# Performance work log

Measured on AMD Instinct MI355X. Metric: run time of the kernel, lower is better.

The kernel has to match this reference:

```python
import jax, jax.numpy as jnp
import numpy as np

DIM = 768
HEADS = 12
HEAD_DIM = DIM // HEADS
MLP_DIM = 4 * DIM
EPS = 1e-5


def setup_inputs() -> dict:
    key = jax.random.key(0)
    ks = jax.random.split(key, 8)
    s = lambda fan_in: 1.0 / np.sqrt(fan_in)
    return {
        "x": jax.random.normal(ks[0], (2, 2048, DIM), dtype=jnp.float32),
        "ln1_w": jnp.ones((DIM,), jnp.float32),
        "ln1_b": jnp.zeros((DIM,), jnp.float32),
        # weights stored [in, out]
        "qkv_w": jax.random.normal(ks[1], (DIM, 3 * DIM), jnp.float32) * s(DIM),
        "qkv_b": jnp.zeros((3 * DIM,), jnp.float32),
        "proj_w": jax.random.normal(ks[2], (DIM, DIM), jnp.float32) * s(DIM),
        "proj_b": jnp.zeros((DIM,), jnp.float32),
        "ln2_w": jnp.ones((DIM,), jnp.float32),
        "ln2_b": jnp.zeros((DIM,), jnp.float32),
        "lin1_w": jax.random.normal(ks[3], (DIM, MLP_DIM), jnp.float32) * s(DIM),
        "lin1_b": jnp.zeros((MLP_DIM,), jnp.float32),
        "lin2_w": jax.random.normal(ks[4], (MLP_DIM, DIM), jnp.float32) * s(MLP_DIM),
        "lin2_b": jnp.zeros((DIM,), jnp.float32),
    }


def _layernorm(x, w, b):
    mu = jnp.mean(x, axis=-1, keepdims=True)
    var = jnp.mean(jnp.square(x - mu), axis=-1, keepdims=True)
    return (x - mu) * jax.lax.rsqrt(var + EPS) * w + b


def _attention(x, qkv_w, qkv_b, proj_w, proj_b):
    B, N, C = x.shape
    qkv = (x @ qkv_w + qkv_b).reshape(B, N, 3, HEADS, HEAD_DIM)
    q, k, v = qkv[:, :, 0], qkv[:, :, 1], qkv[:, :, 2]  # [B, N, H, Dh]
    scale = HEAD_DIM ** -0.5
    attn = jnp.einsum("bqhd,bkhd->bhqk", q, k) * scale  # full NxN scores
    attn = jax.nn.softmax(attn, axis=-1)
    out = jnp.einsum("bhqk,bkhd->bqhd", attn, v).reshape(B, N, C)
    return out @ proj_w + proj_b


def reference(x, ln1_w, ln1_b, qkv_w, qkv_b, proj_w, proj_b,
              ln2_w, ln2_b, lin1_w, lin1_b, lin2_w, lin2_b):
    x = x + _attention(_layernorm(x, ln1_w, ln1_b), qkv_w, qkv_b, proj_w, proj_b)
    h = _layernorm(x, ln2_w, ln2_b)
    h = jax.nn.gelu(h @ lin1_w + lin1_b, approximate=False) @ lin2_w + lin2_b
    return x + h
```

## Files before the change

kernel.cpp:

```cpp
#include <hip/hip_runtime.h>
#include <hip/hip_bf16.h>
#include <math.h>

#define DIM 768
#define NTOK 4096
#define SEQ 2048
#define HEADS 12
#define HD 64

using bf16x8 = __attribute__((ext_vector_type(8))) __bf16;
using bf16x4 = __attribute__((ext_vector_type(4))) __bf16;
using short4v = __attribute__((ext_vector_type(4))) short;
using f32x4  = __attribute__((ext_vector_type(4))) float;
typedef unsigned short u16;

#define KEXPF 0.18033688011112042f

__device__ inline u16 f2bf(float f) {
  union { float f; unsigned u; } v; v.f = f;
  unsigned r = v.u + 0x7fffu + ((v.u >> 16) & 1u);
  return (u16)(r >> 16);
}

__device__ inline void pk2bf(float a, float b, u16* o0, u16* o1) {
  union { __hip_bfloat162 h; u16 u[2]; } cv;
  cv.h = __float22bfloat162_rn(make_float2(a, b));
  *o0 = cv.u[0];
  *o1 = cv.u[1];
}

__device__ inline unsigned pku32(float a, float b) {
  union { __hip_bfloat162 h; unsigned u; } cv;
  cv.h = __float22bfloat162_rn(make_float2(a, b));
  return cv.u;
}

__device__ inline float gelu_t(float x) {
  float z = x * (1.5957691216f + 0.0713548162f * x * x);
  return x / (1.0f + __expf(-z));
}

__device__ inline void gl_lds16(const u16* g, u16* l) {
  __builtin_amdgcn_global_load_lds(
      (const __attribute__((address_space(1))) unsigned int*)g,
      (__attribute__((address_space(3))) unsigned int*)l, 16, 0, 0);
}

__global__ __launch_bounds__(256) void ln_kernel(const float* __restrict__ x,
                                                 const float* __restrict__ w,
                                                 const float* __restrict__ b,
                                                 u16* __restrict__ y) {
  int row = blockIdx.x;
  int t = threadIdx.x;
  const float* xr = x + (size_t)row * DIM;
  float v0 = xr[t], v1 = xr[t + 256], v2 = xr[t + 512];
  float s = v0 + v1 + v2;
  float q = v0 * v0 + v1 * v1 + v2 * v2;
  for (int o = 32; o > 0; o >>= 1) {
    s += __shfl_down(s, o, 64);
    q += __shfl_down(q, o, 64);
  }
  __shared__ float ws_[4], wq_[4], mb[2];
  int wid = t >> 6;
  if ((t & 63) == 0) { ws_[wid] = s; wq_[wid] = q; }
  __syncthreads();
  if (t == 0) {
    float S = ws_[0] + ws_[1] + ws_[2] + ws_[3];
    float Q = wq_[0] + wq_[1] + wq_[2] + wq_[3];
    float mean = S * (1.0f / DIM);
    float var = Q * (1.0f / DIM) - mean * mean;
    mb[0] = mean;
    mb[1] = rsqrtf(var + 1e-5f);
  }
  __syncthreads();
  float mean = mb[0], rstd = mb[1];
  u16* yr = y + (size_t)row * DIM;
  yr[t]       = f2bf((v0 - mean) * rstd * w[t]       + b[t]);
  yr[t + 256] = f2bf((v1 - mean) * rstd * w[t + 256] + b[t + 256]);
  yr[t + 512] = f2bf((v2 - mean) * rstd * w[t + 512] + b[t + 512]);
}

__global__ __launch_bounds__(256) void redln_kernel(
    const float* __restrict__ P0, const float* __restrict__ P1,
    const float* __restrict__ bias, const float* __restrict__ res,
    float* __restrict__ x2, const float* __restrict__ lnw,
    const float* __restrict__ lnb, u16* __restrict__ y) {
  int row = blockIdx.x;
  int t = threadIdx.x;
  size_t off = (size_t)row * DIM;
  float v[3];
#pragma unroll
  for (int k = 0; k < 3; ++k) {
    int c = t + k * 256;
    v[k] = P0[off + c] + P1[off + c] + bias[c] + res[off + c];
    x2[off + c] = v[k];
  }
  float s = v[0] + v[1] + v[2];
  float q = v[0] * v[0] + v[1] * v[1] + v[2] * v[2];
  for (int o = 32; o > 0; o >>= 1) {
    s += __shfl_down(s, o, 64);
    q += __shfl_down(q, o, 64);
  }
  __shared__ float ws_[4], wq_[4], mb[2];
  int wid = t >> 6;
  if ((t & 63) == 0) { ws_[wid] = s; wq_[wid] = q; }
  __syncthreads();
  if (t == 0) {
    float S = ws_[0] + ws_[1] + ws_[2] + ws_[3];
    float Q = wq_[0] + wq_[1] + wq_[2] + wq_[3];
    float mean = S * (1.0f / DIM);
    float var = Q * (1.0f / DIM) - mean * mean;
    mb[0] = mean;
    mb[1] = rsqrtf(var + 1e-5f);
  }
  __syncthreads();
  float mean = mb[0], rstd = mb[1];
#pragma unroll
  for (int k = 0; k < 3; ++k) {
    int c = t + k * 256;
    y[off + c] = f2bf((v[k] - mean) * rstd * lnw[c] + lnb[c]);
  }
}

__global__ __launch_bounds__(256) void wcvt_all(
    const float* __restrict__ W0, const float* __restrict__ W1,
    const float* __restrict__ W2, const float* __restrict__ W3,
    u16* __restrict__ T0, u16* __restrict__ T1,
    u16* __restrict__ T2, u16* __restrict__ T3) {
  int id = blockIdx.x;
  const float* W; u16* Wt; int K, N, local;
  if (id < 1728)      { W = W0; Wt = T0; K = 768;  N = 2304; local = id; }
  else if (id < 2304) { W = W1; Wt = T1; K = 768;  N = 768;  local = id - 1728; }
  else if (id < 4608) { W = W2; Wt = T2; K = 768;  N = 3072; local = id - 2304; }
  else                { W = W3; Wt = T3; K = 3072; N = 768;  local = id - 4608; }
  int ntiles = N / 32;
  int n0 = (local % ntiles) * 32, k0 = (local / ntiles) * 32;
  __shared__ float tile[32][33];
  int tid = threadIdx.x;
  int c = tid & 31, r8 = tid >> 5;
#pragma unroll
  for (int p = 0; p < 4; ++p) {
    int k = r8 + p * 8;
    tile[k][c] = W[(size_t)(k0 + k) * N + n0 + c];
  }
  __syncthreads();
#pragma unroll
  for (int p = 0; p < 4; ++p) {
    int n = r8 + p * 8;
    Wt[(size_t)(n0 + n) * K + k0 + c] = f2bf(tile[c][n]);
  }
}

__global__ __launch_bounds__(256) void vtr_kernel(const u16* __restrict__ qkvB,
                                                  u16* __restrict__ vT) {
  __shared__ u16 tile[32][33];
  int v0 = blockIdx.x * 32, j0 = blockIdx.y * 32, b = blockIdx.z;
  int tid = threadIdx.x;
  int c = tid & 31, r8 = tid >> 5;
#pragma unroll
  for (int p = 0; p < 4; ++p) {
    int r = r8 + p * 8;
    tile[r][c] = qkvB[((size_t)(b * SEQ + j0 + r)) * 2304 + 1536 + v0 + c];
  }
  __syncthreads();
#pragma unroll
  for (int p = 0; p < 4; ++p) {
    int r = r8 + p * 8;
    vT[((size_t)(b * 768 + v0 + r)) * SEQ + j0 + c] = tile[c][r];
  }
}

__global__ __launch_bounds__(256) void bgemm_kernel(
    const u16* __restrict__ A, const u16* __restrict__ Bt,
    const float* __restrict__ bias, u16* __restrict__ Cb,
    int M, int N, int K, int act, int scaleq) {
  __shared__ __align__(16) u16 Asl[3][128 * 32];
  __shared__ __align__(16) u16 Bsl[3][128 * 32];
  int nwg = gridDim.x * gridDim.y;
  int bid = blockIdx.y * gridDim.x + blockIdx.x;
  int swz = (bid & 7) * (nwg >> 3) + (bid >> 3);
  int bx = swz % gridDim.x, by = swz / gridDim.x;
  int tid = threadIdx.x;
  int lane = tid & 63, wave = tid >> 6;
  int wm = wave >> 1, wn = wave & 1;
  int bm = by * 128, bn = bx * 128;
  int l15 = lane & 15, quad = lane >> 4;
  int srow4 = lane >> 2;
  int gux = (lane & 3) ^ ((srow4 + (srow4 >> 2)) & 3);

  f32x4 acc[4][4] = {};
  const u16* Ap = A + (size_t)(bm + wave * 16 + srow4) * K + gux * 8;
  const u16* Bp = Bt + (size_t)(bn + wave * 16 + srow4) * K + gux * 8;
  int fx = (l15 + (l15 >> 2)) & 3;
  int nk = K >> 5;

  auto STAGE = [&](int k0, int sel) {
#pragma unroll
    for (int p = 0; p < 2; ++p)
      gl_lds16(Ap + (size_t)(p * 64) * K + k0, &Asl[sel][(wave * 16 + p * 64) * 32]);
#pragma unroll
    for (int p = 0; p < 2; ++p)
      gl_lds16(Bp + (size_t)(p * 64) * K + k0, &Bsl[sel][(wave * 16 + p * 64) * 32]);
  };

  STAGE(0, 0);
  STAGE(32, 1);
  STAGE(64, 2);
  asm volatile("s_waitcnt vmcnt(8)" ::: "memory");
  __builtin_amdgcn_s_barrier();

  int sel = 0;
  for (int t = 0; t < nk; ++t) {
    bf16x8 af[4], bfr[4];
#pragma unroll
    for (int i = 0; i < 4; ++i) {
      af[i]  = *(const bf16x8*)&Asl[sel][(wm * 64 + i * 16 + l15) * 32 + (quad ^ fx) * 8];
      bfr[i] = *(const bf16x8*)&Bsl[sel][(wn * 64 + i * 16 + l15) * 32 + (quad ^ fx) * 8];
    }
#pragma unroll
    for (int i = 0; i < 4; ++i)
#pragma unroll
      for (int j = 0; j < 4; ++j)
        acc[i][j] = __builtin_amdgcn_mfma_f32_16x16x32_bf16(af[i], bfr[j], acc[i][j], 0, 0, 0);
    if (t == nk - 1) break;
    __builtin_amdgcn_sched_barrier(0);
    __builtin_amdgcn_s_barrier();
    __builtin_amdgcn_sched_barrier(0);
    if (t + 3 < nk) {
      STAGE((t + 3) << 5, sel);
      asm volatile("s_waitcnt vmcnt(8)" ::: "memory");
    } else if (t + 2 < nk) {
      asm volatile("s_waitcnt vmcnt(4)" ::: "memory");
    } else {
      asm volatile("s_waitcnt vmcnt(0)" ::: "memory");
    }
    __builtin_amdgcn_sched_barrier(0);
    __builtin_amdgcn_s_barrier();
    __builtin_amdgcn_sched_barrier(0);
    sel = (sel == 2) ? 0 : sel + 1;
  }

#pragma unroll
  for (int i = 0; i < 4; ++i) {
#pragma unroll
    for (int j = 0; j < 4; ++j) {
      int n = bn + wn * 64 + j * 16 + l15;
      float bv = bias[n];
      float cs = (scaleq && n < 768) ? KEXPF : 1.0f;
      float val[4];
#pragma unroll
      for (int r = 0; r < 4; ++r) {
        float v = (acc[i][j][r] + bv) * cs;
        val[r] = act ? gelu_t(v) : v;
      }
      u16 c0, c1, c2, c3;
      pk2bf(val[0], val[1], &c0, &c1);
      pk2bf(val[2], val[3], &c2, &c3);
      size_t mbase = (size_t)(bm + wm * 64 + i * 16 + quad * 4) * N + n;
      Cb[mbase]         = c0;
      Cb[mbase + N]     = c1;
      Cb[mbase + 2 * N] = c2;
      Cb[mbase + 3 * N] = c3;
    }
  }
}

__global__ __launch_bounds__(256) void bgemm_splitk(
    const u16* __restrict__ A, const u16* __restrict__ Bt,
    float* __restrict__ P0, float* __restrict__ P1,
    int M, int N, int K) {
  __shared__ __align__(16) u16 Asl[2][128 * 64];
  __shared__ __align__(16) u16 Bsl[2][64 * 64];
  int nwg = gridDim.x * gridDim.y;
  int bid = blockIdx.y * gridDim.x + blockIdx.x;
  int swz = (bid & 7) * (nwg >> 3) + (bid >> 3);
  int bx = swz % gridDim.x, by = swz / gridDim.x;
  int tid = threadIdx.x;
  int lane = tid & 63, wave = tid >> 6;
  int wm = wave >> 1, wn = wave & 1;
  int bm = by * 128, bn = bx * 64;
  int l15 = lane & 15, quad = lane >> 4;
  int sm8 = tid >> 3;
  int kgx = (tid & 7) ^ (sm8 & 7);
  int half = K >> 1;
  int kbeg = blockIdx.z * half;

  f32x4 acc[4][2] = {};
  const u16* Ap = A + (size_t)(bm + sm8) * K + kbeg + kgx * 8;
  const u16* Bp = Bt + (size_t)(bn + sm8) * K + kbeg + kgx * 8;
  int xr = l15 & 7;
  int nk = half >> 6;

  auto STAGE = [&](int k0, int sel) {
#pragma unroll
    for (int p = 0; p < 4; ++p)
      gl_lds16(Ap + (size_t)(p * 32) * K + k0, &Asl[sel][(wave * 8 + p * 32) * 64]);
#pragma unroll
    for (int p = 0; p < 2; ++p)
      gl_lds16(Bp + (size_t)(p * 32) * K + k0, &Bsl[sel][(wave * 8 + p * 32) * 64]);
  };

  STAGE(0, 0);
  if (nk > 1) STAGE(64, 1);
  asm volatile("s_waitcnt vmcnt(6)" ::: "memory");
  __builtin_amdgcn_s_barrier();

  for (int t = 0; t < nk; ++t) {
    int sel = t & 1;
#pragma unroll
    for (int ks = 0; ks < 2; ++ks) {
      int pu = ((ks << 2) + quad) ^ xr;
      bf16x8 af[4], bfr[2];
#pragma unroll
      for (int i = 0; i < 4; ++i)
        af[i] = *(const bf16x8*)&Asl[sel][(wm * 64 + i * 16 + l15) * 64 + pu * 8];
#pragma unroll
      for (int j = 0; j < 2; ++j)
        bfr[j] = *(const bf16x8*)&Bsl[sel][(wn * 32 + j * 16 + l15) * 64 + pu * 8];
#pragma unroll
      for (int i = 0; i < 4; ++i)
#pragma unroll
        for (int j = 0; j < 2; ++j)
          acc[i][j] = __builtin_amdgcn_mfma_f32_16x16x32_bf16(af[i], bfr[j], acc[i][j], 0, 0, 0);
    }
    if (t == nk - 1) break;
    __builtin_amdgcn_sched_barrier(0);
    __builtin_amdgcn_s_barrier();
    __builtin_amdgcn_sched_barrier(0);
    if (t + 2 < nk) {
      STAGE((t + 2) << 6, sel);
      asm volatile("s_waitcnt vmcnt(6)" ::: "memory");
    } else {
      asm volatile("s_waitcnt vmcnt(0)" ::: "memory");
    }
    __builtin_amdgcn_sched_barrier(0);
    __builtin_amdgcn_s_barrier();
    __builtin_amdgcn_sched_barrier(0);
  }

  float* P = blockIdx.z ? P1 : P0;
#pragma unroll
  for (int i = 0; i < 4; ++i) {
#pragma unroll
    for (int j = 0; j < 2; ++j) {
      int n = bn + wn * 32 + j * 16 + l15;
#pragma unroll
      for (int r = 0; r < 4; ++r) {
        int m = bm + wm * 64 + i * 16 + quad * 4 + r;
        P[(size_t)m * N + n] = acc[i][j][r];
      }
    }
  }
}

__global__ __launch_bounds__(256) void red_kernel(
    const float* P0, const float* __restrict__ P1,
    const float* __restrict__ bias, const float* __restrict__ res,
    float* O, int Ncols) {
  int i = blockIdx.x * 256 + threadIdx.x;
  float4 a = ((const float4*)P0)[i];
  float4 b = ((const float4*)P1)[i];
  float4 r = ((const float4*)res)[i];
  int col = (i * 4) % Ncols;
  float4 bi = *(const float4*)&bias[col];
  float4 o;
  o.x = a.x + b.x + r.x + bi.x;
  o.y = a.y + b.y + r.y + bi.y;
  o.z = a.z + b.z + r.z + bi.z;
  o.w = a.w + b.w + r.w + bi.w;
  ((float4*)O)[i] = o;
}

#define LDP 68
__global__ __launch_bounds__(256, 3) void attn_kernel(const u16* __restrict__ qkv,
                                                      const u16* __restrict__ vT,
                                                      u16* __restrict__ out) {
  __shared__ __align__(16) char arena[40960];
  u16* Qsp = (u16*)arena;
  u16* Ksp = (u16*)(arena + 8192);
  u16* Vsp = (u16*)(arena + 24576);

  int nwg = gridDim.x * gridDim.y * gridDim.z;
  int bid = (blockIdx.z * gridDim.y + blockIdx.y) * gridDim.x + blockIdx.x;
  int swz = (bid & 7) * (nwg >> 3) + (bid >> 3);
  int bx = swz % gridDim.x;
  int rem = swz / gridDim.x;
  int h = rem % gridDim.y, b = rem / gridDim.y;

  int tid = threadIdx.x;
  int lane = tid & 63, wave = tid >> 6;
  int l15 = lane & 15, quad = lane >> 4;
  int qt = bx * 64;
  size_t base = (size_t)b * SEQ;
  int srow = lane >> 3;
  int sux = (lane & 7) ^ (srow & 7);
  int r0 = wave * 16;
  const u16* qbase = qkv + (base + qt) * 2304 + h * HD;
  const u16* kbase = qkv + base * 2304 + 768 + h * HD;
  const u16* vbase = vT + ((size_t)(b * HEADS + h) * HD) * SEQ;

  gl_lds16(qbase + (size_t)(r0 + srow) * 2304 + sux * 8, Qsp + r0 * 64);
  gl_lds16(qbase + (size_t)(r0 + 8 + srow) * 2304 + sux * 8, Qsp + (r0 + 8) * 64);
  gl_lds16(kbase + (size_t)(r0 + srow) * 2304 + sux * 8, Ksp + r0 * 64);
  gl_lds16(kbase + (size_t)(r0 + 8 + srow) * 2304 + sux * 8, Ksp + (r0 + 8) * 64);
  gl_lds16(vbase + (size_t)(r0 + srow) * SEQ + sux * 8, Vsp + r0 * 64);
  gl_lds16(vbase + (size_t)(r0 + 8 + srow) * SEQ + sux * 8, Vsp + (r0 + 8) * 64);
  __syncthreads();

  int xr = l15 & 7;
  bf16x8 qf[4][2];
#pragma unroll
  for (int g = 0; g < 4; ++g)
#pragma unroll
    for (int s = 0; s < 2; ++s)
      qf[g][s] = *(const bf16x8*)&Qsp[(g * 16 + l15) * 64 + ((s * 4 + quad) ^ xr) * 8];

  gl_lds16(kbase + (size_t)(64 + r0 + srow) * 2304 + sux * 8, Ksp + 4096 + r0 * 64);
  gl_lds16(kbase + (size_t)(64 + r0 + 8 + srow) * 2304 + sux * 8, Ksp + 4096 + (r0 + 8) * 64);
  gl_lds16(vbase + (size_t)(r0 + srow) * SEQ + 64 + sux * 8, Vsp + 4096 + r0 * 64);
  gl_lds16(vbase + (size_t)(r0 + 8 + srow) * SEQ + 64 + sux * 8, Vsp + 4096 + (r0 + 8) * 64);

  int koff0 = (wave * 16 + l15) * 64 + ((quad ^ xr)) * 8;
  int koff1 = (wave * 16 + l15) * 64 + (((4 + quad) ^ xr)) * 8;
  int voff[4];
#pragma unroll
  for (int dg = 0; dg < 4; ++dg)
    voff[dg] = (dg * 16 + l15) * 64 + (((2 * wave + (quad >> 1)) ^ xr)) * 8 + (quad & 1) * 4;

  f32x4 oT[4][4] = {};
  f32x4 oT1[4] = {};
  const short4v ONES = {(short)0x3F80, (short)0x3F80, (short)0x3F80, (short)0x3F80};
  int buf = 0;

  for (int t = 0; t < 32; ++t) {
    const u16* Kb = Ksp + buf * 4096;
    const u16* Vb = Vsp + buf * 4096;

    f32x4 sT[4] = {};
    __builtin_amdgcn_s_setprio(1);
    {
      bf16x8 ak = *(const bf16x8*)&Kb[koff0];
#pragma unroll
      for (int g = 0; g < 4; ++g)
        sT[g] = __builtin_amdgcn_mfma_f32_16x16x32_bf16(ak, qf[g][0], sT[g], 0, 0, 0);
      bf16x8 ak1 = *(const bf16x8*)&Kb[koff1];
#pragma unroll
      for (int g = 0; g < 4; ++g)
        sT[g] = __builtin_amdgcn_mfma_f32_16x16x32_bf16(ak1, qf[g][1], sT[g], 0, 0, 0);
    }
    __builtin_amdgcn_s_setprio(0);

    short4v pb[4];
#pragma unroll
    for (int g = 0; g < 4; ++g) {
      float p0 = __builtin_amdgcn_exp2f(sT[g][0]);
      float p1 = __builtin_amdgcn_exp2f(sT[g][1]);
      float p2 = __builtin_amdgcn_exp2f(sT[g][2]);
      float p3 = __builtin_amdgcn_exp2f(sT[g][3]);
      union { unsigned u[2]; short4v s; } cv;
      cv.u[0] = pku32(p0, p1);
      cv.u[1] = pku32(p2, p3);
      pb[g] = cv.s;
    }

    short4v av[4];
#pragma unroll
    for (int dg = 0; dg < 4; ++dg)
      av[dg] = *(const short4v*)&Vb[voff[dg]];
    __builtin_amdgcn_s_setprio(1);
#pragma unroll
    for (int dg = 0; dg < 4; ++dg)
#pragma unroll
      for (int g = 0; g < 4; ++g)
        oT[dg][g] = __builtin_amdgcn_mfma_f32_16x16x16bf16_1k(av[dg], pb[g], oT[dg][g], 0, 0, 0);
#pragma unroll
    for (int g = 0; g < 4; ++g)
      oT1[g] = __builtin_amdgcn_mfma_f32_16x16x16bf16_1k(ONES, pb[g], oT1[g], 0, 0, 0);
    __builtin_amdgcn_s_setprio(0);

    __builtin_amdgcn_sched_barrier(0);
    __builtin_amdgcn_s_barrier();
    __builtin_amdgcn_sched_barrier(0);
    if (t < 30) {
      size_t kt2 = (size_t)(t + 2) * 64;
      u16* Kd = Ksp + buf * 4096;
      u16* Vd = Vsp + buf * 4096;
      gl_lds16(kbase + (kt2 + r0 + srow) * 2304 + sux * 8, Kd + r0 * 64);
      gl_lds16(kbase + (kt2 + r0 + 8 + srow) * 2304 + sux * 8, Kd + (r0 + 8) * 64);
      gl_lds16(vbase + (size_t)(r0 + srow) * SEQ + kt2 + sux * 8, Vd + r0 * 64);
      gl_lds16(vbase + (size_t)(r0 + 8 + srow) * SEQ + kt2 + sux * 8, Vd + (r0 + 8) * 64);
      asm volatile("s_waitcnt vmcnt(4)" ::: "memory");
    } else {
      asm volatile("s_waitcnt vmcnt(0)" ::: "memory");
    }
    __builtin_amdgcn_sched_barrier(0);
    __builtin_amdgcn_s_barrier();
    __builtin_amdgcn_sched_barrier(0);
    buf ^= 1;
  }

  float* LDSw = (float*)arena;
  float* lsd  = (float*)(arena + 17408);
  if (lane < 16) {
#pragma unroll
    for (int g = 0; g < 4; ++g) lsd[wave * 64 + g * 16 + lane] = oT1[g][0];
  }
  float linv = 0.f;
#pragma unroll
  for (int dg = 0; dg < 4; ++dg) {
#pragma unroll
    for (int g = 0; g < 4; ++g)
#pragma unroll
      for (int r = 0; r < 4; ++r)
        LDSw[wave * (16 * LDP) + (quad * 4 + r) * LDP + g * 16 + l15] = oT[dg][g][r];
    __syncthreads();
    if (dg == 0) {
      float L = lsd[wave * 16 + l15] + lsd[64 + wave * 16 + l15] +
                lsd[128 + wave * 16 + l15] + lsd[192 + wave * 16 + l15];
      linv = 1.0f / L;
    }
    float sv[4];
#pragma unroll
    for (int i = 0; i < 4; ++i) {
      int dloc = quad * 4 + i;
      float a = LDSw[dloc * LDP + wave * 16 + l15] +
                LDSw[1 * (16 * LDP) + dloc * LDP + wave * 16 + l15] +
                LDSw[2 * (16 * LDP) + dloc * LDP + wave * 16 + l15] +
                LDSw[3 * (16 * LDP) + dloc * LDP + wave * 16 + l15];
      sv[i] = a * linv;
    }
    size_t addr = (base + qt + wave * 16 + l15) * DIM + h * HD + dg * 16 + quad * 4;
    uint2 pk;
    pk.x = pku32(sv[0], sv[1]);
    pk.y = pku32(sv[2], sv[3]);
    *(uint2*)&out[addr] = pk;
    __syncthreads();
  }
}

extern "C" void kernel_launch(void* const* d_in, const int* in_sizes, int n_in,
                              void* d_out, int out_size, void* d_ws, size_t ws_size,
                              hipStream_t stream) {
  const float* x     = (const float*)d_in[0];
  const float* ln1w  = (const float*)d_in[1];
  const float* ln1b  = (const float*)d_in[2];
  const float* qkvw  = (const float*)d_in[3];
  const float* qkvbi = (const float*)d_in[4];
  const float* projw = (const float*)d_in[5];
  const float* projb = (const float*)d_in[6];
  const float* ln2w  = (const float*)d_in[7];
  const float* ln2b  = (const float*)d_in[8];
  const float* l1w   = (const float*)d_in[9];
  const float* l1b   = (const float*)d_in[10];
  const float* l2w   = (const float*)d_in[11];
  const float* l2b   = (const float*)d_in[12];
  float* out = (float*)d_out;

  char* w = (char*)d_ws;
  u16*   h     = (u16*)w;   w += (size_t)NTOK * DIM * 2;
  u16*   qkvB  = (u16*)w;
  u16*   mid   = (u16*)w;   w += (size_t)NTOK * 3072 * 2;
  u16*   attnb = (u16*)w;   w += (size_t)NTOK * DIM * 2;
  float* x2    = (float*)w; w += (size_t)NTOK * DIM * 4;
  u16*   vTb   = (u16*)w;   w += (size_t)NTOK * DIM * 2;
  u16*   qkvwt = (u16*)w;   w += (size_t)DIM * 2304 * 2;
  u16*   projwt= (u16*)w;   w += (size_t)DIM * DIM * 2;
  u16*   l1wt  = (u16*)w;   w += (size_t)DIM * 3072 * 2;
  u16*   l2wt  = (u16*)w;   w += (size_t)3072 * DIM * 2;
  float* Pbuf  = (float*)w; w += (size_t)NTOK * DIM * 4;

  wcvt_all<<<6912, 256, 0, stream>>>(qkvw, projw, l1w, l2w,
                                     qkvwt, projwt, l1wt, l2wt);

  ln_kernel<<<NTOK, 256, 0, stream>>>(x, ln1w, ln1b, h);
  bgemm_kernel<<<dim3(2304 / 128, NTOK / 128), 256, 0, stream>>>(
      h, qkvwt, qkvbi, qkvB, NTOK, 2304, DIM, 0, 1);
  vtr_kernel<<<dim3(768 / 32, SEQ / 32, 2), 256, 0, stream>>>(qkvB, vTb);
  attn_kernel<<<dim3(SEQ / 64, HEADS, 2), 256, 0, stream>>>(qkvB, vTb, attnb);

  bgemm_splitk<<<dim3(DIM / 64, NTOK / 128, 2), 256, 0, stream>>>(
      attnb, projwt, x2, Pbuf, NTOK, DIM, DIM);
  redln_kernel<<<NTOK, 256, 0, stream>>>(x2, Pbuf, projb, x, x2, ln2w, ln2b, h);

  bgemm_kernel<<<dim3(3072 / 128, NTOK / 128), 256, 0, stream>>>(
      h, l1wt, l1b, mid, NTOK, 3072, DIM, 1, 0);

  bgemm_splitk<<<dim3(DIM / 64, NTOK / 128, 2), 256, 0, stream>>>(
      mid, l2wt, out, Pbuf, NTOK, DIM, 3072);
  red_kernel<<<NTOK * DIM / 1024, 256, 0, stream>>>(out, Pbuf, l2b, x2, out, DIM);
}
```

Before: 269.8 us.

## Split attention work across 8 waves with query-half by key-slice partition

The attention kernel now runs with 512 threads (8 waves) instead of 256. Each wave handles half of the 64 query rows and one 16-key slice, which halves the per-wave accumulators and Q fragments. The tile loads are spread across more waves, each issuing half as many. The epilogue reduction through LDS is reorganised to match: a new padded layout and 4-byte output stores. The aim is more waves resident per CU with lower register pressure, to hide latency better. The cost is more cross-wave reduction traffic and more barrier participants.

```diff
diff --git a/kernel.cpp b/kernel.cpp
--- a/kernel.cpp
+++ b/kernel.cpp
@@ -371,8 +371,8 @@
   ((float4*)O)[i] = o;
 }
 
-#define LDP 68
-__global__ __launch_bounds__(256, 3) void attn_kernel(const u16* __restrict__ qkv,
+#define LQP 33
+__global__ __launch_bounds__(512, 6) void attn_kernel(const u16* __restrict__ qkv,
                                                       const u16* __restrict__ vT,
                                                       u16* __restrict__ out) {
   __shared__ __align__(16) char arena[40960];
@@ -389,46 +389,42 @@
 
   int tid = threadIdx.x;
   int lane = tid & 63, wave = tid >> 6;
+  int ws = wave & 1, js = wave >> 1;
   int l15 = lane & 15, quad = lane >> 4;
   int qt = bx * 64;
   size_t base = (size_t)b * SEQ;
   int srow = lane >> 3;
   int sux = (lane & 7) ^ (srow & 7);
-  int r0 = wave * 16;
+  int r0 = wave * 8;
   const u16* qbase = qkv + (base + qt) * 2304 + h * HD;
   const u16* kbase = qkv + base * 2304 + 768 + h * HD;
   const u16* vbase = vT + ((size_t)(b * HEADS + h) * HD) * SEQ;
 
   gl_lds16(qbase + (size_t)(r0 + srow) * 2304 + sux * 8, Qsp + r0 * 64);
-  gl_lds16(qbase + (size_t)(r0 + 8 + srow) * 2304 + sux * 8, Qsp + (r0 + 8) * 64);
   gl_lds16(kbase + (size_t)(r0 + srow) * 2304 + sux * 8, Ksp + r0 * 64);
-  gl_lds16(kbase + (size_t)(r0 + 8 + srow) * 2304 + sux * 8, Ksp + (r0 + 8) * 64);
   gl_lds16(vbase + (size_t)(r0 + srow) * SEQ + sux * 8, Vsp + r0 * 64);
-  gl_lds16(vbase + (size_t)(r0 + 8 + srow) * SEQ + sux * 8, Vsp + (r0 + 8) * 64);
   __syncthreads();
 
   int xr = l15 & 7;
-  bf16x8 qf[4][2];
-#pragma unroll
-  for (int g = 0; g < 4; ++g)
+  bf16x8 qf[2][2];
+#pragma unroll
+  for (int g = 0; g < 2; ++g)
 #pragma unroll
     for (int s = 0; s < 2; ++s)
-      qf[g][s] = *(const bf16x8*)&Qsp[(g * 16 + l15) * 64 + ((s * 4 + quad) ^ xr) * 8];
+      qf[g][s] = *(const bf16x8*)&Qsp[(ws * 32 + g * 16 + l15) * 64 + ((s * 4 + quad) ^ xr) * 8];
 
   gl_lds16(kbase + (size_t)(64 + r0 + srow) * 2304 + sux * 8, Ksp + 4096 + r0 * 64);
-  gl_lds16(kbase + (size_t)(64 + r0 + 8 + srow) * 2304 + sux * 8, Ksp + 4096 + (r0 + 8) * 64);
   gl_lds16(vbase + (size_t)(r0 + srow) * SEQ + 64 + sux * 8, Vsp + 4096 + r0 * 64);
-  gl_lds16(vbase + (size_t)(r0 + 8 + srow) * SEQ + 64 + sux * 8, Vsp + 4096 + (r0 + 8) * 64);
-
-  int koff0 = (wave * 16 + l15) * 64 + ((quad ^ xr)) * 8;
-  int koff1 = (wave * 16 + l15) * 64 + (((4 + quad) ^ xr)) * 8;
+
+  int koff0 = (js * 16 + l15) * 64 + ((quad ^ xr)) * 8;
+  int koff1 = (js * 16 + l15) * 64 + (((4 + quad) ^ xr)) * 8;
   int voff[4];
 #pragma unroll
   for (int dg = 0; dg < 4; ++dg)
-    voff[dg] = (dg * 16 + l15) * 64 + (((2 * wave + (quad >> 1)) ^ xr)) * 8 + (quad & 1) * 4;
-
-  f32x4 oT[4][4] = {};
-  f32x4 oT1[4] = {};
+    voff[dg] = (dg * 16 + l15) * 64 + (((2 * js + (quad >> 1)) ^ xr)) * 8 + (quad & 1) * 4;
+
+  f32x4 oT[4][2] = {};
+  f32x4 oT1[2] = {};
   const short4v ONES = {(short)0x3F80, (short)0x3F80, (short)0x3F80, (short)0x3F80};
   int buf = 0;
 
@@ -436,23 +432,23 @@
     const u16* Kb = Ksp + buf * 4096;
     const u16* Vb = Vsp + buf * 4096;
 
-    f32x4 sT[4] = {};
+    f32x4 sT[2] = {};
     __builtin_amdgcn_s_setprio(1);
     {
       bf16x8 ak = *(const bf16x8*)&Kb[koff0];
 #pragma unroll
-      for (int g = 0; g < 4; ++g)
+      for (int g = 0; g < 2; ++g)
         sT[g] = __builtin_amdgcn_mfma_f32_16x16x32_bf16(ak, qf[g][0], sT[g], 0, 0, 0);
       bf16x8 ak1 = *(const bf16x8*)&Kb[koff1];
 #pragma unroll
-      for (int g = 0; g < 4; ++g)
+      for (int g = 0; g < 2; ++g)
         sT[g] = __builtin_amdgcn_mfma_f32_16x16x32_bf16(ak1, qf[g][1], sT[g], 0, 0, 0);
     }
     __builtin_amdgcn_s_setprio(0);
 
-    short4v pb[4];
-#pragma unroll
-    for (int g = 0; g < 4; ++g) {
+    short4v pb[2];
+#pragma unroll
+    for (int g = 0; g < 2; ++g) {
       float p0 = __builtin_amdgcn_exp2f(sT[g][0]);
       float p1 = __builtin_amdgcn_exp2f(sT[g][1]);
       float p2 = __builtin_amdgcn_exp2f(sT[g][2]);
@@ -471,10 +467,10 @@
 #pragma unroll
     for (int dg = 0; dg < 4; ++dg)
 #pragma unroll
-      for (int g = 0; g < 4; ++g)
+      for (int g = 0; g < 2; ++g)
         oT[dg][g] = __builtin_amdgcn_mfma_f32_16x16x16bf16_1k(av[dg], pb[g], oT[dg][g], 0, 0, 0);
 #pragma unroll
-    for (int g = 0; g < 4; ++g)
+    for (int g = 0; g < 2; ++g)
       oT1[g] = __builtin_amdgcn_mfma_f32_16x16x16bf16_1k(ONES, pb[g], oT1[g], 0, 0, 0);
     __builtin_amdgcn_s_setprio(0);
 
@@ -486,10 +482,8 @@
       u16* Kd = Ksp + buf * 4096;
       u16* Vd = Vsp + buf * 4096;
       gl_lds16(kbase + (kt2 + r0 + srow) * 2304 + sux * 8, Kd + r0 * 64);
-      gl_lds16(kbase + (kt2 + r0 + 8 + srow) * 2304 + sux * 8, Kd + (r0 + 8) * 64);
       gl_lds16(vbase + (size_t)(r0 + srow) * SEQ + kt2 + sux * 8, Vd + r0 * 64);
-      gl_lds16(vbase + (size_t)(r0 + 8 + srow) * SEQ + kt2 + sux * 8, Vd + (r0 + 8) * 64);
-      asm volatile("s_waitcnt vmcnt(4)" ::: "memory");
+      asm volatile("s_waitcnt vmcnt(2)" ::: "memory");
     } else {
       asm volatile("s_waitcnt vmcnt(0)" ::: "memory");
     }
@@ -503,37 +497,37 @@
   float* lsd  = (float*)(arena + 17408);
   if (lane < 16) {
 #pragma unroll
-    for (int g = 0; g < 4; ++g) lsd[wave * 64 + g * 16 + lane] = oT1[g][0];
-  }
+    for (int g = 0; g < 2; ++g)
+      lsd[(ws * 4 + js) * 32 + g * 16 + lane] = oT1[g][0];
+  }
+  int qq = tid & 63, dd2 = tid >> 6;
+  int ws2 = qq >> 5, qx = qq & 31;
   float linv = 0.f;
 #pragma unroll
   for (int dg = 0; dg < 4; ++dg) {
 #pragma unroll
-    for (int g = 0; g < 4; ++g)
+    for (int g = 0; g < 2; ++g)
 #pragma unroll
       for (int r = 0; r < 4; ++r)
-        LDSw[wave * (16 * LDP) + (quad * 4 + r) * LDP + g * 16 + l15] = oT[dg][g][r];
+        LDSw[((ws * 4 + js) * 16 + quad * 4 + r) * LQP + g * 16 + l15] = oT[dg][g][r];
     __syncthreads();
     if (dg == 0) {
-      float L = lsd[wave * 16 + l15] + lsd[64 + wave * 16 + l15] +
-                lsd[128 + wave * 16 + l15] + lsd[192 + wave * 16 + l15];
+      float L = lsd[(ws2 * 4 + 0) * 32 + qx] + lsd[(ws2 * 4 + 1) * 32 + qx] +
+                lsd[(ws2 * 4 + 2) * 32 + qx] + lsd[(ws2 * 4 + 3) * 32 + qx];
       linv = 1.0f / L;
     }
-    float sv[4];
-#pragma unroll
-    for (int i = 0; i < 4; ++i) {
-      int dloc = quad * 4 + i;
-      float a = LDSw[dloc * LDP + wave * 16 + l15] +
-                LDSw[1 * (16 * LDP) + dloc * LDP + wave * 16 + l15] +
-                LDSw[2 * (16 * LDP) + dloc * LDP + wave * 16 + l15] +
-                LDSw[3 * (16 * LDP) + dloc * LDP + wave * 16 + l15];
-      sv[i] = a * linv;
-    }
-    size_t addr = (base + qt + wave * 16 + l15) * DIM + h * HD + dg * 16 + quad * 4;
-    uint2 pk;
-    pk.x = pku32(sv[0], sv[1]);
-    pk.y = pku32(sv[2], sv[3]);
-    *(uint2*)&out[addr] = pk;
+    float sv[2];
+#pragma unroll
+    for (int hlf = 0; hlf < 2; ++hlf) {
+      int dloc = dd2 * 2 + hlf;
+      float a = LDSw[((ws2 * 4 + 0) * 16 + dloc) * LQP + qx] +
+                LDSw[((ws2 * 4 + 1) * 16 + dloc) * LQP + qx] +
+                LDSw[((ws2 * 4 + 2) * 16 + dloc) * LQP + qx] +
+                LDSw[((ws2 * 4 + 3) * 16 + dloc) * LQP + qx];
+      sv[hlf] = a * linv;
+    }
+    size_t addr = (base + qt + qq) * DIM + h * HD + dg * 16 + dd2 * 2;
+    *(unsigned*)&out[addr] = pku32(sv[0], sv[1]);
     __syncthreads();
   }
 }
@@ -576,7 +570,7 @@
   bgemm_kernel<<<dim3(2304 / 128, NTOK / 128), 256, 0, stream>>>(
       h, qkvwt, qkvbi, qkvB, NTOK, 2304, DIM, 0, 1);
   vtr_kernel<<<dim3(768 / 32, SEQ / 32, 2), 256, 0, stream>>>(qkvB, vTb);
-  attn_kernel<<<dim3(SEQ / 64, HEADS, 2), 256, 0, stream>>>(qkvB, vTb, attnb);
+  attn_kernel<<<dim3(SEQ / 64, HEADS, 2), 512, 0, stream>>>(qkvB, vTb, attnb);
 
   bgemm_splitk<<<dim3(DIM / 64, NTOK / 128, 2), 256, 0, stream>>>(
       attnb, projwt, x2, Pbuf, NTOK, DIM, DIM);
```

New measurement: 266.6 us. About the same (-1.2%).
